# Optimization experiments

Hardware: AMD Instinct MI355X
Metric: run time of the kernel (lower is better)

Reference implementation:

```python
import jax, jax.numpy as jnp
import numpy as np

D_MODEL = 1024
N_HEADS = 16
K_RETRIEVED = 32
BANK_SIZE = 131072
EPS = 1e-12  # matches F.normalize eps


def setup_inputs() -> dict:
    key = jax.random.key(0)
    ks = jax.random.split(key, 7)
    B, T = 8, 2048
    x = jax.random.normal(ks[0], (B, T, D_MODEL), dtype=jnp.float32)
    mem_keys = jax.random.normal(ks[1], (BANK_SIZE, D_MODEL), dtype=jnp.float32)
    mem_values = jax.random.normal(ks[2], (BANK_SIZE, D_MODEL), dtype=jnp.float32)
    s = 1.0 / np.sqrt(D_MODEL)
    Wq = jax.random.normal(ks[3], (D_MODEL, D_MODEL), dtype=jnp.float32) * s
    Wk = jax.random.normal(ks[4], (D_MODEL, D_MODEL), dtype=jnp.float32) * s
    Wv = jax.random.normal(ks[5], (D_MODEL, D_MODEL), dtype=jnp.float32) * s
    Wo = jax.random.normal(ks[6], (D_MODEL, D_MODEL), dtype=jnp.float32) * s
    gate_logit = jnp.zeros((1,), dtype=jnp.float32)
    return {"x": x, "mem_keys": mem_keys, "mem_values": mem_values,
            "Wq": Wq, "Wk": Wk, "Wv": Wv, "Wo": Wo, "gate_logit": gate_logit}


def _normalize(v):
    n = jnp.linalg.norm(v, axis=-1, keepdims=True)
    return v / jnp.maximum(n, EPS)


def reference(x, mem_keys, mem_values, Wq, Wk, Wv, Wo, gate_logit):
    B, T, D = x.shape
    H, hd, k = N_HEADS, D_MODEL // N_HEADS, K_RETRIEVED

    # --- retrieval: mean-pool query, cosine-sim top-k, gather values ---
    q = x.mean(axis=1)                       # (B, D)
    sims = _normalize(q) @ _normalize(mem_keys).T   # (B, BANK_SIZE)
    _, idx = jax.lax.top_k(sims, k)          # (B, k) descending
    retrieved = mem_values[idx]              # (B, k, d_mem)

    # --- cross-attention over retrieved docs ---
    Q = (x @ Wq).reshape(B, T, H, hd)
    K = (retrieved @ Wk).reshape(B, k, H, hd)
    V = (retrieved @ Wv).reshape(B, k, H, hd)
    scale = 1.0 / jnp.sqrt(jnp.asarray(hd, dtype=x.dtype))
    attn = jnp.einsum('bthd,bkhd->bhtk', Q, K) * scale
    attn = jax.nn.softmax(attn, axis=-1)
    ctx = jnp.einsum('bhtk,bkhd->bthd', attn, V).reshape(B, T, D)
    ctx = ctx @ Wo

    gate = jax.nn.sigmoid(gate_logit)        # (1,) broadcasts
    return x + gate * ctx
```

## Files before the change

kernel.cpp:

```cpp
#include <hip/hip_runtime.h>

#define D_MODEL 1024
#define NH 16
#define HD 64
#define KRET 32
#define BANK 131072
#define BB 8
#define TT 2048
#define MTOK 16384
#define EPSN 1e-12f

typedef __attribute__((ext_vector_type(8))) short bf16x8;
typedef __attribute__((ext_vector_type(4))) float f32x4;

__device__ __forceinline__ unsigned short f2bf(float f) {
  unsigned int u = __float_as_uint(f);
  u += 0x7fffu + ((u >> 16) & 1u);
  return (unsigned short)(u >> 16);
}
__device__ __forceinline__ float bf2f(unsigned short h) {
  return __uint_as_float(((unsigned int)h) << 16);
}

__device__ __forceinline__ void gload16(const void* g, void* l) {
  __builtin_amdgcn_global_load_lds(
      (const __attribute__((address_space(1))) unsigned int*)g,
      (__attribute__((address_space(3))) unsigned int*)l, 16, 0, 0);
}

__global__ __launch_bounds__(256) void k_conv_bf16(const float* __restrict__ in,
                                                   unsigned short* __restrict__ out, int n4) {
  int i = blockIdx.x * 256 + threadIdx.x;
  if (i >= n4) return;
  float4 v = ((const float4*)in)[i];
  ushort4 o;
  o.x = f2bf(v.x); o.y = f2bf(v.y); o.z = f2bf(v.z); o.w = f2bf(v.w);
  ((ushort4*)out)[i] = o;
}

__global__ __launch_bounds__(256) void k_transW(const float* W0, const float* W1,
                                                const float* W2, const float* W3,
                                                unsigned short* T0, unsigned short* T1,
                                                unsigned short* T2, unsigned short* T3) {
  const float* W; unsigned short* T;
  switch (blockIdx.z) {
    case 0: W = W0; T = T0; break;
    case 1: W = W1; T = T1; break;
    case 2: W = W2; T = T2; break;
    default: W = W3; T = T3; break;
  }
  __shared__ float tile[64][65];
  int k0 = blockIdx.y * 64, n0 = blockIdx.x * 64;
  int tid = threadIdx.x;
#pragma unroll
  for (int i = 0; i < 16; i++) {
    int idx = tid + i * 256; int r = idx >> 6, c = idx & 63;
    tile[r][c] = W[(size_t)(k0 + r) * D_MODEL + n0 + c];
  }
  __syncthreads();
#pragma unroll
  for (int i = 0; i < 16; i++) {
    int idx = tid + i * 256; int r = idx >> 6, c = idx & 63;
    T[(size_t)(n0 + r) * D_MODEL + k0 + c] = f2bf(tile[c][r]);
  }
}

__global__ __launch_bounds__(256) void k_meanpart(const float* __restrict__ x,
                                                  float* __restrict__ part) {
  int b = blockIdx.z, tc = blockIdx.y;
  int d = blockIdx.x * 256 + threadIdx.x;
  const float* xp = x + ((size_t)b * TT + tc * 256) * D_MODEL + d;
  float s = 0.f;
  for (int t = 0; t < 256; t++) s += xp[(size_t)t * D_MODEL];
  part[((size_t)b * 8 + tc) * D_MODEL + d] = s;
}

__global__ __launch_bounds__(256) void k_qnorm(const float* __restrict__ part,
                                               float* __restrict__ qn) {
  int b = blockIdx.x; int tid = threadIdx.x;
  __shared__ float qs[D_MODEL];
  __shared__ float red[4];
  float ss = 0.f;
#pragma unroll
  for (int c = 0; c < 4; c++) {
    int d = c * 256 + tid;
    float s = 0.f;
#pragma unroll
    for (int p = 0; p < 8; p++) s += part[((size_t)b * 8 + p) * D_MODEL + d];
    s *= (1.f / TT);
    qs[d] = s; ss += s * s;
  }
#pragma unroll
  for (int m = 32; m >= 1; m >>= 1) ss += __shfl_xor(ss, m);
  if ((tid & 63) == 0) red[tid >> 6] = ss;
  __syncthreads();
  float tot = red[0] + red[1] + red[2] + red[3];
  float inv = 1.f / fmaxf(sqrtf(tot), EPSN);
#pragma unroll
  for (int c = 0; c < 4; c++) {
    int d = c * 256 + tid;
    qn[(size_t)b * D_MODEL + d] = qs[d] * inv;
  }
}

__global__ __launch_bounds__(256) void k_sims(const float* __restrict__ mk,
                                              const float* __restrict__ qn,
                                              float* __restrict__ sims) {
  int wave = threadIdx.x >> 6, lane = threadIdx.x & 63;
  int row0 = (blockIdx.x * 4 + wave) * 4;
  float4 kv[4][4];
#pragma unroll
  for (int r = 0; r < 4; r++) {
    const float4* kr = (const float4*)(mk + (size_t)(row0 + r) * D_MODEL);
#pragma unroll
    for (int i = 0; i < 4; i++) kv[r][i] = kr[lane + 64 * i];
  }
  float ss[4] = {0.f, 0.f, 0.f, 0.f};
#pragma unroll
  for (int r = 0; r < 4; r++)
#pragma unroll
    for (int i = 0; i < 4; i++)
      ss[r] += kv[r][i].x * kv[r][i].x + kv[r][i].y * kv[r][i].y +
               kv[r][i].z * kv[r][i].z + kv[r][i].w * kv[r][i].w;
  float dots[8][4];
#pragma unroll
  for (int b = 0; b < 8; b++)
#pragma unroll
    for (int r = 0; r < 4; r++) dots[b][r] = 0.f;
#pragma unroll
  for (int b = 0; b < 8; b++) {
    const float4* qb = (const float4*)(qn + (size_t)b * D_MODEL);
#pragma unroll
    for (int i = 0; i < 4; i++) {
      float4 q4 = qb[lane + 64 * i];
#pragma unroll
      for (int r = 0; r < 4; r++)
        dots[b][r] += kv[r][i].x * q4.x + kv[r][i].y * q4.y +
                      kv[r][i].z * q4.z + kv[r][i].w * q4.w;
    }
  }
#pragma unroll
  for (int m = 32; m >= 1; m >>= 1) {
#pragma unroll
    for (int r = 0; r < 4; r++) ss[r] += __shfl_xor(ss[r], m);
#pragma unroll
    for (int b = 0; b < 8; b++)
#pragma unroll
      for (int r = 0; r < 4; r++) dots[b][r] += __shfl_xor(dots[b][r], m);
  }
  if (lane == 0) {
#pragma unroll
    for (int r = 0; r < 4; r++) {
      float inv = 1.f / fmaxf(sqrtf(ss[r]), EPSN);
#pragma unroll
      for (int b = 0; b < 8; b++)
        sims[(size_t)b * BANK + row0 + r] = dots[b][r] * inv;
    }
  }
}

__global__ __launch_bounds__(256) void k_topk_local(const float* __restrict__ sims,
                                                    float* __restrict__ cval,
                                                    int* __restrict__ cidx) {
  int b = blockIdx.y, chunk = blockIdx.x;
  int tid = threadIdx.x, wave = tid >> 6, lane = tid & 63;
  const float* sb = sims + (size_t)b * BANK + chunk * 2048;
  float v[8]; int gi[8];
#pragma unroll
  for (int j = 0; j < 8; j++) {
    int loc = j * 256 + tid;
    v[j] = sb[loc];
    gi[j] = chunk * 2048 + loc;
  }
  __shared__ float wv[4]; __shared__ int wi[4];
  __shared__ int bcast;
  for (int it = 0; it < KRET; ++it) {
    float best = -1e30f; int besti = 1 << 30;
#pragma unroll
    for (int j = 0; j < 8; j++)
      if (v[j] > best || (v[j] == best && gi[j] < besti)) { best = v[j]; besti = gi[j]; }
#pragma unroll
    for (int m = 32; m >= 1; m >>= 1) {
      float ov = __shfl_xor(best, m); int oi = __shfl_xor(besti, m);
      if (ov > best || (ov == best && oi < besti)) { best = ov; besti = oi; }
    }
    if (lane == 0) { wv[wave] = best; wi[wave] = besti; }
    __syncthreads();
    if (tid == 0) {
      float fb = wv[0]; int fi = wi[0];
      for (int w = 1; w < 4; w++)
        if (wv[w] > fb || (wv[w] == fb && wi[w] < fi)) { fb = wv[w]; fi = wi[w]; }
      bcast = fi;
      cval[((size_t)b * 64 + chunk) * KRET + it] = fb;
      cidx[((size_t)b * 64 + chunk) * KRET + it] = fi;
    }
    __syncthreads();
    int w = bcast;
#pragma unroll
    for (int j = 0; j < 8; j++)
      if (gi[j] == w) v[j] = -1e30f;
  }
}

__global__ __launch_bounds__(256) void k_topk_merge(const float* __restrict__ cval,
                                                    const int* __restrict__ cidx,
                                                    int* __restrict__ idx) {
  int b = blockIdx.x;
  int tid = threadIdx.x, wave = tid >> 6, lane = tid & 63;
  const float* cv = cval + (size_t)b * 2048;
  const int* ci = cidx + (size_t)b * 2048;
  float v[8]; int gi[8];
#pragma unroll
  for (int j = 0; j < 8; j++) {
    int loc = j * 256 + tid;
    v[j] = cv[loc];
    gi[j] = ci[loc];
  }
  __shared__ float wv[4]; __shared__ int wi[4];
  __shared__ int bcast;
  for (int it = 0; it < KRET; ++it) {
    float best = -1e30f; int besti = 1 << 30;
#pragma unroll
    for (int j = 0; j < 8; j++)
      if (v[j] > best || (v[j] == best && gi[j] < besti)) { best = v[j]; besti = gi[j]; }
#pragma unroll
    for (int m = 32; m >= 1; m >>= 1) {
      float ov = __shfl_xor(best, m); int oi = __shfl_xor(besti, m);
      if (ov > best || (ov == best && oi < besti)) { best = ov; besti = oi; }
    }
    if (lane == 0) { wv[wave] = best; wi[wave] = besti; }
    __syncthreads();
    if (tid == 0) {
      float fb = wv[0]; int fi = wi[0];
      for (int w = 1; w < 4; w++)
        if (wv[w] > fb || (wv[w] == fb && wi[w] < fi)) { fb = wv[w]; fi = wi[w]; }
      bcast = fi;
      idx[b * KRET + it] = fi;
    }
    __syncthreads();
    int w = bcast;
#pragma unroll
    for (int j = 0; j < 8; j++)
      if (gi[j] == w) v[j] = -1e30f;
  }
}

__global__ __launch_bounds__(256) void k_gather(const float* __restrict__ mv,
                                                const int* __restrict__ idx,
                                                unsigned short* __restrict__ retr) {
  int row = blockIdx.x;
  int src = idx[row];
  float4 v = ((const float4*)(mv + (size_t)src * D_MODEL))[threadIdx.x];
  ushort4 o;
  o.x = f2bf(v.x); o.y = f2bf(v.y); o.z = f2bf(v.z); o.w = f2bf(v.w);
  ((ushort4*)(retr + (size_t)row * D_MODEL))[threadIdx.x] = o;
}

template <int MODE>
__global__ __launch_bounds__(256) void k_gemm(const unsigned short* __restrict__ A,
                                              const unsigned short* __restrict__ Bt,
                                              float* __restrict__ out_f,
                                              unsigned short* __restrict__ out_b,
                                              float* __restrict__ out_f2,
                                              const float* __restrict__ xres,
                                              const float* __restrict__ gatep) {
  __shared__ __align__(16) unsigned short As[128 * 32];
  __shared__ __align__(16) unsigned short Bs[128 * 32];
  const int tid = threadIdx.x;
  const int wave = tid >> 6, lane = tid & 63;
  const int bm = blockIdx.x * 128, bn = blockIdx.y * 128;
  const int wm = (wave >> 1) * 64, wn = (wave & 1) * 64;
  const int frow = lane & 15, kg = lane >> 4;
  const int K = 1024;

  f32x4 acc[4][4] = {};

  const int g0 = tid * 8;
  const int g1 = 2048 + tid * 8;
  const unsigned short* a0 = A + (size_t)(bm + (g0 >> 5)) * K + (g0 & 31);
  const unsigned short* a1 = A + (size_t)(bm + (g1 >> 5)) * K + (g1 & 31);
  const unsigned short* b0 = Bt + (size_t)(bn + (g0 >> 5)) * K + (g0 & 31);
  const unsigned short* b1 = Bt + (size_t)(bn + (g1 >> 5)) * K + (g1 & 31);
  unsigned short* lA0 = &As[wave * 512];
  unsigned short* lA1 = &As[2048 + wave * 512];
  unsigned short* lB0 = &Bs[wave * 512];
  unsigned short* lB1 = &Bs[2048 + wave * 512];

  for (int k0 = 0; k0 < K; k0 += 32) {
    gload16(a0 + k0, lA0);
    gload16(a1 + k0, lA1);
    gload16(b0 + k0, lB0);
    gload16(b1 + k0, lB1);
    __syncthreads();
    bf16x8 fa[4], fb[4];
#pragma unroll
    for (int i = 0; i < 4; i++)
      fa[i] = *(const bf16x8*)&As[(wm + i * 16 + frow) * 32 + kg * 8];
#pragma unroll
    for (int i = 0; i < 4; i++)
      fb[i] = *(const bf16x8*)&Bs[(wn + i * 16 + frow) * 32 + kg * 8];
#pragma unroll
    for (int i = 0; i < 4; i++)
#pragma unroll
      for (int j = 0; j < 4; j++)
        acc[i][j] = __builtin_amdgcn_mfma_f32_16x16x32_bf16(fa[i], fb[j], acc[i][j], 0, 0, 0);
    __syncthreads();
  }

  const int crow = (lane >> 4) * 4, ccol = lane & 15;
  if (MODE == 2) {
    float gate = 1.f / (1.f + __expf(-gatep[0]));
#pragma unroll
    for (int i = 0; i < 4; i++)
#pragma unroll
      for (int j = 0; j < 4; j++)
#pragma unroll
        for (int r = 0; r < 4; r++) {
          int gm = bm + wm + i * 16 + crow + r;
          int gn = bn + wn + j * 16 + ccol;
          size_t off = (size_t)gm * D_MODEL + gn;
          out_f[off] = xres[off] + gate * acc[i][j][r];
        }
  } else if (MODE == 0) {
#pragma unroll
    for (int i = 0; i < 4; i++)
#pragma unroll
      for (int j = 0; j < 4; j++)
#pragma unroll
        for (int r = 0; r < 4; r++) {
          int gm = bm + wm + i * 16 + crow + r;
          int gn = bn + wn + j * 16 + ccol;
          int b = gm >> 11, t = gm & 2047, h = gn >> 6, d = gn & 63;
          out_b[((((size_t)b * NH + h) * TT + t) << 6) + d] = f2bf(acc[i][j][r]);
        }
  } else {
#pragma unroll
    for (int i = 0; i < 4; i++)
#pragma unroll
      for (int j = 0; j < 4; j++)
#pragma unroll
        for (int r = 0; r < 4; r++) {
          int gm = bm + wm + i * 16 + crow + r;
          int gn = bn + wn + j * 16 + ccol;
          int b = gm >> 5, jj = gm & 31;
          if (gn < 1024) {
            int h = gn >> 6, d = gn & 63;
            out_f[((((size_t)b * NH + h) * KRET + jj) << 6) + d] = acc[i][j][r];
          } else {
            int gn2 = gn - 1024;
            int h = gn2 >> 6, d = gn2 & 63;
            out_f2[((((size_t)b * NH + h) * KRET + jj) << 6) + d] = acc[i][j][r];
          }
        }
  }
}

__global__ __launch_bounds__(256) void k_attn(const unsigned short* __restrict__ Qb,
                                              const float* __restrict__ Kws,
                                              const float* __restrict__ Vws,
                                              unsigned short* __restrict__ ctx) {
  __shared__ __align__(16) float Ks[KRET * HD];
  __shared__ __align__(16) float Vs[KRET * HD];
  int bh = blockIdx.y; int b = bh >> 4, h = bh & 15;
  int tid = threadIdx.x;
  int t = blockIdx.x * 256 + tid;
  const float4* kp = (const float4*)(Kws + (size_t)bh * KRET * HD);
  const float4* vp = (const float4*)(Vws + (size_t)bh * KRET * HD);
  ((float4*)Ks)[tid] = kp[tid];
  ((float4*)Ks)[tid + 256] = kp[tid + 256];
  ((float4*)Vs)[tid] = vp[tid];
  ((float4*)Vs)[tid + 256] = vp[tid + 256];
  __syncthreads();

  const uint4* qp = (const uint4*)(Qb + ((size_t)bh * TT + t) * HD);
  float q[64];
#pragma unroll
  for (int i = 0; i < 8; i++) {
    uint4 u = qp[i];
    unsigned vals[4] = {u.x, u.y, u.z, u.w};
#pragma unroll
    for (int w = 0; w < 4; w++) {
      q[i * 8 + w * 2 + 0] = bf2f((unsigned short)(vals[w] & 0xffffu));
      q[i * 8 + w * 2 + 1] = bf2f((unsigned short)(vals[w] >> 16));
    }
  }
  float s[KRET];
#pragma unroll
  for (int j = 0; j < KRET; j++) {
    const float4* kr = (const float4*)&Ks[j * HD];
    float a = 0.f;
#pragma unroll
    for (int d4 = 0; d4 < 16; d4++) {
      float4 kk = kr[d4];
      a += q[d4 * 4 + 0] * kk.x + q[d4 * 4 + 1] * kk.y +
           q[d4 * 4 + 2] * kk.z + q[d4 * 4 + 3] * kk.w;
    }
    s[j] = a * 0.125f;
  }
  float m = s[0];
#pragma unroll
  for (int j = 1; j < KRET; j++) m = fmaxf(m, s[j]);
  float sum = 0.f;
#pragma unroll
  for (int j = 0; j < KRET; j++) { s[j] = __expf(s[j] - m); sum += s[j]; }
  float inv = 1.f / sum;
  float o[64];
#pragma unroll
  for (int d = 0; d < 64; d++) o[d] = 0.f;
#pragma unroll
  for (int j = 0; j < KRET; j++) {
    float p = s[j] * inv;
    const float4* vr = (const float4*)&Vs[j * HD];
#pragma unroll
    for (int d4 = 0; d4 < 16; d4++) {
      float4 vv = vr[d4];
      o[d4 * 4 + 0] += p * vv.x; o[d4 * 4 + 1] += p * vv.y;
      o[d4 * 4 + 2] += p * vv.z; o[d4 * 4 + 3] += p * vv.w;
    }
  }
  unsigned short* cp = ctx + ((size_t)(b * TT + t)) * D_MODEL + h * HD;
#pragma unroll
  for (int d4 = 0; d4 < 16; d4++) {
    ushort4 w4;
    w4.x = f2bf(o[d4 * 4 + 0]); w4.y = f2bf(o[d4 * 4 + 1]);
    w4.z = f2bf(o[d4 * 4 + 2]); w4.w = f2bf(o[d4 * 4 + 3]);
    ((ushort4*)cp)[d4] = w4;
  }
}

extern "C" void kernel_launch(void* const* d_in, const int* in_sizes, int n_in,
                              void* d_out, int out_size, void* d_ws, size_t ws_size,
                              hipStream_t stream) {
  const float* x = (const float*)d_in[0];
  const float* mk = (const float*)d_in[1];
  const float* mv = (const float*)d_in[2];
  const float* Wq = (const float*)d_in[3];
  const float* Wk = (const float*)d_in[4];
  const float* Wv = (const float*)d_in[5];
  const float* Wo = (const float*)d_in[6];
  const float* gatep = (const float*)d_in[7];
  float* out = (float*)d_out;

  char* ws = (char*)d_ws;
  unsigned short* xb   = (unsigned short*)(ws);
  unsigned short* Qb   = (unsigned short*)(ws + 33554432);
  unsigned short* WqT  = (unsigned short*)(ws + 67108864);
  unsigned short* WkvT = (unsigned short*)(ws + 69206016);
  unsigned short* WoT  = (unsigned short*)(ws + 73400320);
  float* qpart = (float*)(ws + 75497472);
  float* cval  = (float*)(ws + 75497472);
  int*   cidxb = (int*)(ws + 75497472 + 65536);
  float* qn    = (float*)(ws + 75759616);
  float* sims  = (float*)(ws + 75792384);
  int*   idx   = (int*)(ws + 79986688);
  unsigned short* retr = (unsigned short*)(ws + 79987712);
  float* Kws   = (float*)(ws + 80512000);
  float* Vws   = (float*)(ws + 81560576);

  k_conv_bf16<<<dim3(16384), 256, 0, stream>>>(x, xb, MTOK * D_MODEL / 4);
  k_transW<<<dim3(16, 16, 4), 256, 0, stream>>>(Wq, Wk, Wv, Wo,
                                                WqT, WkvT, WkvT + 1048576, WoT);
  k_meanpart<<<dim3(4, 8, 8), 256, 0, stream>>>(x, qpart);
  k_qnorm<<<dim3(8), 256, 0, stream>>>(qpart, qn);
  k_sims<<<dim3(BANK / 16), 256, 0, stream>>>(mk, qn, sims);
  k_topk_local<<<dim3(64, 8), 256, 0, stream>>>(sims, cval, cidxb);
  k_topk_merge<<<dim3(8), 256, 0, stream>>>(cval, cidxb, idx);
  k_gather<<<dim3(256), 256, 0, stream>>>(mv, idx, retr);
  k_gemm<0><<<dim3(128, 8), 256, 0, stream>>>(xb, WqT, nullptr, Qb, nullptr, nullptr, nullptr);
  k_gemm<1><<<dim3(2, 16), 256, 0, stream>>>(retr, WkvT, Kws, nullptr, Vws, nullptr, nullptr);
  k_attn<<<dim3(8, 128), 256, 0, stream>>>(Qb, Kws, Vws, xb);
  k_gemm<2><<<dim3(128, 8), 256, 0, stream>>>(xb, WoT, out, nullptr, nullptr, x, gatep);
}
```

Baseline: 502.0 us.

## Fuse bf16 conversion with mean pooling and gather into KV GEMM

The x-to-bf16 conversion and the token mean partial sums now happen in one kernel, so x is read once for both instead of twice. The qnorm kernel reduces 64 float4 partials per batch. The memory-value gather and bf16 conversion move into a dedicated KV GEMM that loads indexed fp32 rows directly into shared memory, which removes the separate gather kernel and its intermediate buffer. The trade-off is that the KV GEMM now uses synchronous register loads for A, and the mean-reduction workspace is aliased onto the sims buffer.

```diff
diff --git a/kernel.cpp b/kernel.cpp
--- a/kernel.cpp
+++ b/kernel.cpp
@@ -11,6 +11,7 @@
 #define EPSN 1e-12f
 
 typedef __attribute__((ext_vector_type(8))) short bf16x8;
+typedef __attribute__((ext_vector_type(8))) unsigned short u16x8;
 typedef __attribute__((ext_vector_type(4))) float f32x4;
 
 __device__ __forceinline__ unsigned short f2bf(float f) {
@@ -28,14 +29,22 @@
       (__attribute__((address_space(3))) unsigned int*)l, 16, 0, 0);
 }
 
-__global__ __launch_bounds__(256) void k_conv_bf16(const float* __restrict__ in,
-                                                   unsigned short* __restrict__ out, int n4) {
-  int i = blockIdx.x * 256 + threadIdx.x;
-  if (i >= n4) return;
-  float4 v = ((const float4*)in)[i];
-  ushort4 o;
-  o.x = f2bf(v.x); o.y = f2bf(v.y); o.z = f2bf(v.z); o.w = f2bf(v.w);
-  ((ushort4*)out)[i] = o;
+__global__ __launch_bounds__(256) void k_conv_mean(const float* __restrict__ x,
+                                                   unsigned short* __restrict__ xb,
+                                                   float* __restrict__ part) {
+  int ch = blockIdx.x, b = blockIdx.y, tid = threadIdx.x;
+  const float4* xp = (const float4*)(x + ((size_t)b * TT + ch * 32) * D_MODEL);
+  ushort4* xo = (ushort4*)(xb + ((size_t)b * TT + ch * 32) * D_MODEL);
+  float4 acc = {0.f, 0.f, 0.f, 0.f};
+#pragma unroll 4
+  for (int t = 0; t < 32; t++) {
+    float4 v = xp[t * 256 + tid];
+    acc.x += v.x; acc.y += v.y; acc.z += v.z; acc.w += v.w;
+    ushort4 o;
+    o.x = f2bf(v.x); o.y = f2bf(v.y); o.z = f2bf(v.z); o.w = f2bf(v.w);
+    xo[t * 256 + tid] = o;
+  }
+  ((float4*)part)[((size_t)b * 64 + ch) * 256 + tid] = acc;
 }
 
 __global__ __launch_bounds__(256) void k_transW(const float* W0, const float* W1,
@@ -65,42 +74,28 @@
   }
 }
 
-__global__ __launch_bounds__(256) void k_meanpart(const float* __restrict__ x,
-                                                  float* __restrict__ part) {
-  int b = blockIdx.z, tc = blockIdx.y;
-  int d = blockIdx.x * 256 + threadIdx.x;
-  const float* xp = x + ((size_t)b * TT + tc * 256) * D_MODEL + d;
-  float s = 0.f;
-  for (int t = 0; t < 256; t++) s += xp[(size_t)t * D_MODEL];
-  part[((size_t)b * 8 + tc) * D_MODEL + d] = s;
-}
-
 __global__ __launch_bounds__(256) void k_qnorm(const float* __restrict__ part,
                                                float* __restrict__ qn) {
   int b = blockIdx.x; int tid = threadIdx.x;
-  __shared__ float qs[D_MODEL];
   __shared__ float red[4];
-  float ss = 0.f;
-#pragma unroll
-  for (int c = 0; c < 4; c++) {
-    int d = c * 256 + tid;
-    float s = 0.f;
-#pragma unroll
-    for (int p = 0; p < 8; p++) s += part[((size_t)b * 8 + p) * D_MODEL + d];
-    s *= (1.f / TT);
-    qs[d] = s; ss += s * s;
-  }
+  const float4* pp = (const float4*)part + (size_t)b * 64 * 256 + tid;
+  float4 a = {0.f, 0.f, 0.f, 0.f};
+#pragma unroll 8
+  for (int p = 0; p < 64; p++) {
+    float4 v = pp[(size_t)p * 256];
+    a.x += v.x; a.y += v.y; a.z += v.z; a.w += v.w;
+  }
+  const float sc = 1.f / (float)TT;
+  a.x *= sc; a.y *= sc; a.z *= sc; a.w *= sc;
+  float ss = a.x * a.x + a.y * a.y + a.z * a.z + a.w * a.w;
 #pragma unroll
   for (int m = 32; m >= 1; m >>= 1) ss += __shfl_xor(ss, m);
   if ((tid & 63) == 0) red[tid >> 6] = ss;
   __syncthreads();
   float tot = red[0] + red[1] + red[2] + red[3];
   float inv = 1.f / fmaxf(sqrtf(tot), EPSN);
-#pragma unroll
-  for (int c = 0; c < 4; c++) {
-    int d = c * 256 + tid;
-    qn[(size_t)b * D_MODEL + d] = qs[d] * inv;
-  }
+  float4 o = {a.x * inv, a.y * inv, a.z * inv, a.w * inv};
+  ((float4*)qn)[(size_t)b * 256 + tid] = o;
 }
 
 __global__ __launch_bounds__(256) void k_sims(const float* __restrict__ mk,
@@ -245,15 +240,86 @@
   }
 }
 
-__global__ __launch_bounds__(256) void k_gather(const float* __restrict__ mv,
-                                                const int* __restrict__ idx,
-                                                unsigned short* __restrict__ retr) {
-  int row = blockIdx.x;
-  int src = idx[row];
-  float4 v = ((const float4*)(mv + (size_t)src * D_MODEL))[threadIdx.x];
-  ushort4 o;
-  o.x = f2bf(v.x); o.y = f2bf(v.y); o.z = f2bf(v.z); o.w = f2bf(v.w);
-  ((ushort4*)(retr + (size_t)row * D_MODEL))[threadIdx.x] = o;
+__global__ __launch_bounds__(256) void k_kvgemm(const float* __restrict__ mv,
+                                                const int* __restrict__ idx_g,
+                                                const unsigned short* __restrict__ Bt,
+                                                float* __restrict__ Kout,
+                                                float* __restrict__ Vout) {
+  __shared__ __align__(16) unsigned short As[128 * 32];
+  __shared__ __align__(16) unsigned short Bs[128 * 32];
+  __shared__ int idxs[128];
+  const int tid = threadIdx.x;
+  const int wave = tid >> 6, lane = tid & 63;
+  const int bm = blockIdx.x * 128, bn = blockIdx.y * 128;
+  const int wm = (wave >> 1) * 64, wn = (wave & 1) * 64;
+  const int frow = lane & 15, kg = lane >> 4;
+  const int K = 1024;
+
+  if (tid < 128) idxs[tid] = idx_g[bm + tid];
+  __syncthreads();
+
+  f32x4 acc[4][4] = {};
+
+  const int row0 = tid >> 2, col0 = (tid & 3) * 8;
+  const int row1 = row0 + 64;
+  const int g0 = tid * 8;
+  const int g1 = 2048 + tid * 8;
+  const unsigned short* b0 = Bt + (size_t)(bn + (g0 >> 5)) * K + (g0 & 31);
+  const unsigned short* b1 = Bt + (size_t)(bn + (g1 >> 5)) * K + (g1 & 31);
+  unsigned short* lB0 = &Bs[wave * 512];
+  unsigned short* lB1 = &Bs[2048 + wave * 512];
+  const float* src0 = mv + (size_t)idxs[row0] * D_MODEL + col0;
+  const float* src1 = mv + (size_t)idxs[row1] * D_MODEL + col0;
+
+  for (int k0 = 0; k0 < K; k0 += 32) {
+    gload16(b0 + k0, lB0);
+    gload16(b1 + k0, lB1);
+    float4 u0 = *(const float4*)(src0 + k0);
+    float4 w0 = *(const float4*)(src0 + k0 + 4);
+    float4 u1 = *(const float4*)(src1 + k0);
+    float4 w1 = *(const float4*)(src1 + k0 + 4);
+    u16x8 p0, p1;
+    p0[0] = f2bf(u0.x); p0[1] = f2bf(u0.y); p0[2] = f2bf(u0.z); p0[3] = f2bf(u0.w);
+    p0[4] = f2bf(w0.x); p0[5] = f2bf(w0.y); p0[6] = f2bf(w0.z); p0[7] = f2bf(w0.w);
+    p1[0] = f2bf(u1.x); p1[1] = f2bf(u1.y); p1[2] = f2bf(u1.z); p1[3] = f2bf(u1.w);
+    p1[4] = f2bf(w1.x); p1[5] = f2bf(w1.y); p1[6] = f2bf(w1.z); p1[7] = f2bf(w1.w);
+    *(u16x8*)&As[row0 * 32 + col0] = p0;
+    *(u16x8*)&As[row1 * 32 + col0] = p1;
+    __syncthreads();
+    bf16x8 fa[4], fb[4];
+#pragma unroll
+    for (int i = 0; i < 4; i++)
+      fa[i] = *(const bf16x8*)&As[(wm + i * 16 + frow) * 32 + kg * 8];
+#pragma unroll
+    for (int i = 0; i < 4; i++)
+      fb[i] = *(const bf16x8*)&Bs[(wn + i * 16 + frow) * 32 + kg * 8];
+#pragma unroll
+    for (int i = 0; i < 4; i++)
+#pragma unroll
+      for (int j = 0; j < 4; j++)
+        acc[i][j] = __builtin_amdgcn_mfma_f32_16x16x32_bf16(fa[i], fb[j], acc[i][j], 0, 0, 0);
+    __syncthreads();
+  }
+
+  const int crow = (lane >> 4) * 4, ccol = lane & 15;
+#pragma unroll
+  for (int i = 0; i < 4; i++)
+#pragma unroll
+    for (int j = 0; j < 4; j++)
+#pragma unroll
+      for (int r = 0; r < 4; r++) {
+        int gm = bm + wm + i * 16 + crow + r;
+        int gn = bn + wn + j * 16 + ccol;
+        int b = gm >> 5, jj = gm & 31;
+        if (gn < 1024) {
+          int h = gn >> 6, d = gn & 63;
+          Kout[((((size_t)b * NH + h) * KRET + jj) << 6) + d] = acc[i][j][r];
+        } else {
+          int gn2 = gn - 1024;
+          int h = gn2 >> 6, d = gn2 & 63;
+          Vout[((((size_t)b * NH + h) * KRET + jj) << 6) + d] = acc[i][j][r];
+        }
+      }
 }
 
 template <int MODE>
@@ -261,7 +327,6 @@
                                               const unsigned short* __restrict__ Bt,
                                               float* __restrict__ out_f,
                                               unsigned short* __restrict__ out_b,
-                                              float* __restrict__ out_f2,
                                               const float* __restrict__ xres,
                                               const float* __restrict__ gatep) {
   __shared__ __align__(16) unsigned short As[128 * 32];
@@ -321,7 +386,7 @@
           size_t off = (size_t)gm * D_MODEL + gn;
           out_f[off] = xres[off] + gate * acc[i][j][r];
         }
-  } else if (MODE == 0) {
+  } else {
 #pragma unroll
     for (int i = 0; i < 4; i++)
 #pragma unroll
@@ -332,25 +397,6 @@
           int gn = bn + wn + j * 16 + ccol;
           int b = gm >> 11, t = gm & 2047, h = gn >> 6, d = gn & 63;
           out_b[((((size_t)b * NH + h) * TT + t) << 6) + d] = f2bf(acc[i][j][r]);
-        }
-  } else {
-#pragma unroll
-    for (int i = 0; i < 4; i++)
-#pragma unroll
-      for (int j = 0; j < 4; j++)
-#pragma unroll
-        for (int r = 0; r < 4; r++) {
-          int gm = bm + wm + i * 16 + crow + r;
-          int gn = bn + wn + j * 16 + ccol;
-          int b = gm >> 5, jj = gm & 31;
-          if (gn < 1024) {
-            int h = gn >> 6, d = gn & 63;
-            out_f[((((size_t)b * NH + h) * KRET + jj) << 6) + d] = acc[i][j][r];
-          } else {
-            int gn2 = gn - 1024;
-            int h = gn2 >> 6, d = gn2 & 63;
-            out_f2[((((size_t)b * NH + h) * KRET + jj) << 6) + d] = acc[i][j][r];
-          }
         }
   }
 }
@@ -447,27 +493,24 @@
   unsigned short* WqT  = (unsigned short*)(ws + 67108864);
   unsigned short* WkvT = (unsigned short*)(ws + 69206016);
   unsigned short* WoT  = (unsigned short*)(ws + 73400320);
-  float* qpart = (float*)(ws + 75497472);
-  float* cval  = (float*)(ws + 75497472);
-  int*   cidxb = (int*)(ws + 75497472 + 65536);
-  float* qn    = (float*)(ws + 75759616);
-  float* sims  = (float*)(ws + 75792384);
-  int*   idx   = (int*)(ws + 79986688);
-  unsigned short* retr = (unsigned short*)(ws + 79987712);
-  float* Kws   = (float*)(ws + 80512000);
-  float* Vws   = (float*)(ws + 81560576);
-
-  k_conv_bf16<<<dim3(16384), 256, 0, stream>>>(x, xb, MTOK * D_MODEL / 4);
+  float* qn    = (float*)(ws + 75497472);
+  float* sims  = (float*)(ws + 75530240);
+  float* part  = (float*)(ws + 75530240);
+  int*   idx   = (int*)(ws + 79724544);
+  float* cval  = (float*)(ws + 79725568);
+  int*   cidxb = (int*)(ws + 79791104);
+  float* Kws   = (float*)(ws + 79856640);
+  float* Vws   = (float*)(ws + 80905216);
+
+  k_conv_mean<<<dim3(64, 8), 256, 0, stream>>>(x, xb, part);
   k_transW<<<dim3(16, 16, 4), 256, 0, stream>>>(Wq, Wk, Wv, Wo,
                                                 WqT, WkvT, WkvT + 1048576, WoT);
-  k_meanpart<<<dim3(4, 8, 8), 256, 0, stream>>>(x, qpart);
-  k_qnorm<<<dim3(8), 256, 0, stream>>>(qpart, qn);
+  k_qnorm<<<dim3(8), 256, 0, stream>>>(part, qn);
   k_sims<<<dim3(BANK / 16), 256, 0, stream>>>(mk, qn, sims);
   k_topk_local<<<dim3(64, 8), 256, 0, stream>>>(sims, cval, cidxb);
   k_topk_merge<<<dim3(8), 256, 0, stream>>>(cval, cidxb, idx);
-  k_gather<<<dim3(256), 256, 0, stream>>>(mv, idx, retr);
-  k_gemm<0><<<dim3(128, 8), 256, 0, stream>>>(xb, WqT, nullptr, Qb, nullptr, nullptr, nullptr);
-  k_gemm<1><<<dim3(2, 16), 256, 0, stream>>>(retr, WkvT, Kws, nullptr, Vws, nullptr, nullptr);
+  k_kvgemm<<<dim3(2, 16), 256, 0, stream>>>(mv, idx, WkvT, Kws, Vws);
+  k_gemm<0><<<dim3(128, 8), 256, 0, stream>>>(xb, WqT, nullptr, Qb, nullptr, nullptr);
   k_attn<<<dim3(8, 128), 256, 0, stream>>>(Qb, Kws, Vws, xb);
-  k_gemm<2><<<dim3(128, 8), 256, 0, stream>>>(xb, WoT, out, nullptr, nullptr, x, gatep);
-}
+  k_gemm<2><<<dim3(128, 8), 256, 0, stream>>>(xb, WoT, out, nullptr, x, gatep);
+}
```

Result: no change. 505.3 us (+0.7%).
